# Kernel tuning notes

Hardware: AMD Instinct MI355X
Metric: run time of the kernel (lower is better)

The kernel has to match this reference:

```python
import jax, jax.numpy as jnp
import numpy as np

QMAX = 127.0

def setup_inputs() -> dict:
    key = jax.random.key(0)
    kx, kw, ks = jax.random.split(key, 3)
    B, S, D_IN, D_OUT = 4, 2048, 4096, 4096
    x = jax.random.normal(kx, (B, S, D_IN), dtype=jnp.float16)
    # int8 weight buffer, same distribution as torch.randint(-127, 127)
    weight = jax.random.randint(kw, (D_OUT, D_IN), -127, 127, dtype=jnp.int32).astype(jnp.int8)
    # per-output-channel weight scales (fp16 buffer); small positive values
    weight_scales = (jax.random.uniform(ks, (D_OUT,), dtype=jnp.float32) * 0.01 + 1e-4).astype(jnp.float16)
    return {"x": x, "weight": weight, "weight_scales": weight_scales}

def reference(x, weight, weight_scales):
    # x: [B, S, D_in] fp16; weight: [D_out, D_in] int8; weight_scales: [D_out] fp16
    x32 = x.astype(jnp.float32)
    # dynamic per-token absmax quantization: scale = absmax / 127
    absmax = jnp.max(jnp.abs(x32), axis=-1, keepdims=True)      # [B, S, 1]
    x_scales = jnp.maximum(absmax / QMAX, 1e-8)
    q = jnp.round(x32 / x_scales)                                # in [-127, 127]
    q = jnp.clip(q, -QMAX, QMAX).astype(jnp.int8)
    # int8 GEMM accumulated in int32 (cupy.matmul on int32 in the original)
    y = jnp.einsum('bsk,nk->bsn', q.astype(jnp.int32), weight.astype(jnp.int32),
                   preferred_element_type=jnp.int32)             # [B, S, D_out]
    # dequant: per-token activation scale * per-channel weight scale
    y = y.astype(jnp.float32) * x_scales * weight_scales.astype(jnp.float32)[None, None, :]
    return y.astype(jnp.float16)
```

## Files before the change

kernel.cpp:

```cpp
#include <hip/hip_runtime.h>
#include <stdint.h>

typedef int int32x4 __attribute__((ext_vector_type(4)));

constexpr int K_DIM = 4096;
constexpr int N_DIM = 4096;
constexpr float QMAXF = 127.0f;

__global__ __launch_bounds__(256) void quant_rows(const float* __restrict__ x,
                                                  int8_t* __restrict__ q,
                                                  float* __restrict__ scales) {
    const int row = blockIdx.x;
    const int tid = threadIdx.x;
    const size_t base = (size_t)row * K_DIM;

    const float4* xv = reinterpret_cast<const float4*>(x + base);
    float4 v[4];
#pragma unroll
    for (int i = 0; i < 4; ++i) v[i] = xv[tid + 256 * i];

    float m = 0.0f;
#pragma unroll
    for (int i = 0; i < 4; ++i)
        m = fmaxf(m, fmaxf(fmaxf(fabsf(v[i].x), fabsf(v[i].y)),
                           fmaxf(fabsf(v[i].z), fabsf(v[i].w))));
#pragma unroll
    for (int off = 32; off > 0; off >>= 1) m = fmaxf(m, __shfl_xor(m, off));

    __shared__ float wmax[4];
    if ((tid & 63) == 0) wmax[tid >> 6] = m;
    __syncthreads();
    const float am = fmaxf(fmaxf(wmax[0], wmax[1]), fmaxf(wmax[2], wmax[3]));
    const float scale = fmaxf(am * (1.0f / 127.0f), 1e-8f);
    if (tid == 0) scales[row] = scale;
    const float inv = 1.0f / scale;

    int* qw = reinterpret_cast<int*>(q + base);
#pragma unroll
    for (int i = 0; i < 4; ++i) {
        float f0 = fminf(QMAXF, fmaxf(-QMAXF, rintf(v[i].x * inv)));
        float f1 = fminf(QMAXF, fmaxf(-QMAXF, rintf(v[i].y * inv)));
        float f2 = fminf(QMAXF, fmaxf(-QMAXF, rintf(v[i].z * inv)));
        float f3 = fminf(QMAXF, fmaxf(-QMAXF, rintf(v[i].w * inv)));
        int b0 = ((int)f0) & 255, b1 = ((int)f1) & 255;
        int b2 = ((int)f2) & 255, b3 = ((int)f3) & 255;
        qw[tid + 256 * i] = b0 | (b1 << 8) | (b2 << 16) | (b3 << 24);
    }
}

__global__ __launch_bounds__(256) void pack_w(const int* __restrict__ w,
                                              int8_t* __restrict__ w8) {
    const int idx = blockIdx.x * 256 + threadIdx.x;
    const int4 v = reinterpret_cast<const int4*>(w)[idx];
    int packed = (v.x & 255) | ((v.y & 255) << 8) | ((v.z & 255) << 16) | ((v.w & 255) << 24);
    reinterpret_cast<int*>(w8)[idx] = packed;
}

constexpr int BM = 256, BN = 256, BK = 64;
constexpr int NT = K_DIM / BK;

#define GLL(src, dst)                                                          \
    __builtin_amdgcn_global_load_lds(                                          \
        (const __attribute__((address_space(1))) unsigned int*)(src),          \
        (__attribute__((address_space(3))) unsigned int*)(dst), 16, 0, 0)

__global__ __launch_bounds__(512, 2) void w8a8_gemm256(
        const int8_t* __restrict__ A, const int8_t* __restrict__ B,
        const float* __restrict__ asc, const float* __restrict__ wsc,
        float* __restrict__ C, int M) {
    __shared__ int8_t As[4][BM][BK];
    extern __shared__ int8_t Bs_raw[];
    int8_t* Bs = Bs_raw;

    const int tid  = threadIdx.x;
    const int lane = tid & 63;

    const int nwg = gridDim.x;
    const int bid = blockIdx.x;
    const int swz = (bid & 7) * (nwg >> 3) + (bid >> 3);
    const int NB  = N_DIM / BN;
    const int brow = (swz / NB) * BM;
    const int bcol = (swz % NB) * BN;

    const int wm = (tid >> 6) >> 2;
    const int wn = (tid >> 6) & 3;

    const int s0 = tid, s1 = tid + 512;
    const int r0s = s0 >> 2, g0 = (s0 & 3) ^ ((r0s >> 1) & 3);
    const int r1s = s1 >> 2, g1 = (s1 & 3) ^ ((r1s >> 1) & 3);
    const int8_t* gA0 = A + (size_t)(brow + r0s) * K_DIM + g0 * 16;
    const int8_t* gA1 = A + (size_t)(brow + r1s) * K_DIM + g1 * 16;
    const int8_t* gB0 = B + (size_t)(bcol + r0s) * K_DIM + g0 * 16;
    const int8_t* gB1 = B + (size_t)(bcol + r1s) * K_DIM + g1 * 16;
    const int segb0 = (tid >> 6) * 1024;
    const int segb1 = segb0 + 8192;

    const int l15 = lane & 15;
    const int ls  = lane >> 4;
    const int rA  = wm * 128 + l15;
    const int offA = rA * BK + ((ls ^ ((rA >> 1) & 3)) * 16);
    const int rB  = wn * 64 + l15;
    const int offB = rB * BK + ((ls ^ ((rB >> 1) & 3)) * 16);

    int32x4 acc[8][4];
#pragma unroll
    for (int i = 0; i < 8; ++i)
#pragma unroll
        for (int j = 0; j < 4; ++j) acc[i][j] = (int32x4){0, 0, 0, 0};

#pragma unroll
    for (int t = 0; t < 3; ++t) {
        const size_t kk = (size_t)t * BK;
        int8_t* lA = &As[t][0][0];
        int8_t* lB = Bs + t * (BM * BK);
        GLL(gA0 + kk, lA + segb0);
        GLL(gA1 + kk, lA + segb1);
        GLL(gB0 + kk, lB + segb0);
        GLL(gB1 + kk, lB + segb1);
    }
    asm volatile("s_waitcnt vmcnt(8)" ::: "memory");
    __builtin_amdgcn_s_barrier();

    for (int t = 0; t < NT; ++t) {
        const int b = t & 3;
        const int8_t* abuf = &As[b][0][0];
        const int8_t* bbuf = Bs + b * (BM * BK);
        const int   pb  = (t + 3) & 3;
        const size_t kk = (size_t)(t + 3) * BK;
        const bool  pf  = (t + 3 < NT);

        if (pf) {
            int8_t* lA = &As[pb][0][0];
            GLL(gA0 + kk, lA + segb0);
            GLL(gA1 + kk, lA + segb1);
        }
        int32x4 bf[4], af[4];
#pragma unroll
        for (int ni = 0; ni < 4; ++ni)
            bf[ni] = *(const int32x4*)(bbuf + offB + ni * 1024);
#pragma unroll
        for (int mi = 0; mi < 4; ++mi)
            af[mi] = *(const int32x4*)(abuf + offA + mi * 1024);
        __builtin_amdgcn_s_setprio(1);
#pragma unroll
        for (int mi = 0; mi < 4; ++mi)
#pragma unroll
            for (int ni = 0; ni < 4; ++ni)
                acc[mi][ni] = __builtin_amdgcn_mfma_i32_16x16x64_i8(
                    af[mi], bf[ni], acc[mi][ni], 0, 0, 0);
        __builtin_amdgcn_s_setprio(0);
        __builtin_amdgcn_s_barrier();

        if (pf) {
            int8_t* lB = Bs + pb * (BM * BK);
            GLL(gB0 + kk, lB + segb0);
            GLL(gB1 + kk, lB + segb1);
        }
#pragma unroll
        for (int mi = 0; mi < 4; ++mi)
            af[mi] = *(const int32x4*)(abuf + offA + (mi + 4) * 1024);
        __builtin_amdgcn_s_setprio(1);
#pragma unroll
        for (int mi = 0; mi < 4; ++mi)
#pragma unroll
            for (int ni = 0; ni < 4; ++ni)
                acc[mi + 4][ni] = __builtin_amdgcn_mfma_i32_16x16x64_i8(
                    af[mi], bf[ni], acc[mi + 4][ni], 0, 0, 0);
        __builtin_amdgcn_s_setprio(0);

        if (t < NT - 3)       asm volatile("s_waitcnt vmcnt(8)" ::: "memory");
        else if (t == NT - 3) asm volatile("s_waitcnt vmcnt(4)" ::: "memory");
        else                  asm volatile("s_waitcnt vmcnt(0)" ::: "memory");
        __builtin_amdgcn_s_barrier();
    }

    const int c0  = lane & 15;
    const int rr0 = (lane >> 4) * 4;
#pragma unroll
    for (int ni = 0; ni < 4; ++ni) {
        const int col = bcol + wn * 64 + ni * 16 + c0;
        const float ws = wsc[col];
#pragma unroll
        for (int mi = 0; mi < 8; ++mi) {
            const int rowb = brow + wm * 128 + mi * 16 + rr0;
#pragma unroll
            for (int r = 0; r < 4; ++r) {
                const int row = rowb + r;
                float o = (float)acc[mi][ni][r] * asc[row] * ws;
                o = (float)(_Float16)o;
                C[(size_t)row * N_DIM + col] = o;
            }
        }
    }
}

extern "C" void kernel_launch(void* const* d_in, const int* in_sizes, int n_in,
                              void* d_out, int out_size, void* d_ws, size_t ws_size,
                              hipStream_t stream) {
    const float* x   = (const float*)d_in[0];
    const int*   w   = (const int*)d_in[1];
    const float* wsc = (const float*)d_in[2];
    float* out = (float*)d_out;

    const int K = K_DIM;
    const int M = in_sizes[0] / K;
    const int N = N_DIM;

    int8_t* q   = (int8_t*)d_ws;
    int8_t* w8  = (int8_t*)d_ws + (size_t)M * K;
    float*  asc = (float*)((char*)d_ws + (size_t)M * K + (size_t)N * K);

    quant_rows<<<M, 256, 0, stream>>>(x, q, asc);
    pack_w<<<(N * (K / 4)) / 256, 256, 0, stream>>>(w, w8);
    const int grid = (M / BM) * (N / BN);
    w8a8_gemm256<<<grid, 512, 65536, stream>>>(q, w8, asc, wsc, out, M);
}
```

Before: 199.6 us.

## Split GEMM main loop into four phases with next-tile B fragment prefetch

Restructures the int8 MFMA main loop into four sub-phases per K tile. Each phase issues one global-to-LDS load, reads two A fragments, and prefetches one B fragment from the next stage buffer, then runs eight MFMAs. B fragments are now held in registers across iterations (current and next), and the vmcnt waits are retuned to match. The aim is to spread LDS reads and global loads more evenly between the MFMAs and hide LDS latency. The cost is extra register pressure and eight barriers per K tile instead of two.

```diff
diff --git a/kernel.cpp b/kernel.cpp
--- a/kernel.cpp
+++ b/kernel.cpp
@@ -63,6 +63,8 @@
     __builtin_amdgcn_global_load_lds(                                          \
         (const __attribute__((address_space(1))) unsigned int*)(src),          \
         (__attribute__((address_space(3))) unsigned int*)(dst), 16, 0, 0)
+
+#define MFMA_I8(a, b, c) __builtin_amdgcn_mfma_i32_16x16x64_i8((a), (b), (c), 0, 0, 0)
 
 __global__ __launch_bounds__(512, 2) void w8a8_gemm256(
         const int8_t* __restrict__ A, const int8_t* __restrict__ B,
@@ -118,60 +120,54 @@
         GLL(gB0 + kk, lB + segb0);
         GLL(gB1 + kk, lB + segb1);
     }
-    asm volatile("s_waitcnt vmcnt(8)" ::: "memory");
+    asm volatile("s_waitcnt vmcnt(4)" ::: "memory");
     __builtin_amdgcn_s_barrier();
 
+    int32x4 bf_c[4];
+#pragma unroll
+    for (int p = 0; p < 4; ++p)
+        bf_c[p] = *(const int32x4*)(Bs + offB + p * 1024);
+
     for (int t = 0; t < NT; ++t) {
-        const int b = t & 3;
-        const int8_t* abuf = &As[b][0][0];
-        const int8_t* bbuf = Bs + b * (BM * BK);
-        const int   pb  = (t + 3) & 3;
+        const int8_t* abuf  = &As[t & 3][0][0];
+        const int8_t* bnext = Bs + ((t + 1) & 3) * (BM * BK);
+        int8_t* lA = &As[(t + 3) & 3][0][0];
+        int8_t* lB = Bs + ((t + 3) & 3) * (BM * BK);
         const size_t kk = (size_t)(t + 3) * BK;
-        const bool  pf  = (t + 3 < NT);
-
-        if (pf) {
-            int8_t* lA = &As[pb][0][0];
-            GLL(gA0 + kk, lA + segb0);
-            GLL(gA1 + kk, lA + segb1);
+        const bool pf = (t + 3 < NT);
+
+        int32x4 bf_n[4];
+#pragma unroll
+        for (int p = 0; p < 4; ++p) {
+            if (pf) {
+                if      (p == 0) GLL(gA0 + kk, lA + segb0);
+                else if (p == 1) GLL(gA1 + kk, lA + segb1);
+                else if (p == 2) GLL(gB0 + kk, lB + segb0);
+                else             GLL(gB1 + kk, lB + segb1);
+            }
+            int32x4 a0 = *(const int32x4*)(abuf + offA + (2 * p) * 1024);
+            int32x4 a1 = *(const int32x4*)(abuf + offA + (2 * p + 1) * 1024);
+            bf_n[p]    = *(const int32x4*)(bnext + offB + p * 1024);
+
+            __builtin_amdgcn_s_barrier();
+            asm volatile("s_waitcnt lgkmcnt(0)" ::: "memory");
+            __builtin_amdgcn_s_setprio(1);
+#pragma unroll
+            for (int ni = 0; ni < 4; ++ni)
+                acc[2 * p][ni] = MFMA_I8(a0, bf_c[ni], acc[2 * p][ni]);
+#pragma unroll
+            for (int ni = 0; ni < 4; ++ni)
+                acc[2 * p + 1][ni] = MFMA_I8(a1, bf_c[ni], acc[2 * p + 1][ni]);
+            __builtin_amdgcn_s_setprio(0);
+
+            if (p == 3) {
+                if (t < NT - 3) asm volatile("s_waitcnt vmcnt(4)" ::: "memory");
+                else            asm volatile("s_waitcnt vmcnt(0)" ::: "memory");
+            }
+            __builtin_amdgcn_s_barrier();
         }
-        int32x4 bf[4], af[4];
-#pragma unroll
-        for (int ni = 0; ni < 4; ++ni)
-            bf[ni] = *(const int32x4*)(bbuf + offB + ni * 1024);
-#pragma unroll
-        for (int mi = 0; mi < 4; ++mi)
-            af[mi] = *(const int32x4*)(abuf + offA + mi * 1024);
-        __builtin_amdgcn_s_setprio(1);
-#pragma unroll
-        for (int mi = 0; mi < 4; ++mi)
-#pragma unroll
-            for (int ni = 0; ni < 4; ++ni)
-                acc[mi][ni] = __builtin_amdgcn_mfma_i32_16x16x64_i8(
-                    af[mi], bf[ni], acc[mi][ni], 0, 0, 0);
-        __builtin_amdgcn_s_setprio(0);
-        __builtin_amdgcn_s_barrier();
-
-        if (pf) {
-            int8_t* lB = Bs + pb * (BM * BK);
-            GLL(gB0 + kk, lB + segb0);
-            GLL(gB1 + kk, lB + segb1);
-        }
-#pragma unroll
-        for (int mi = 0; mi < 4; ++mi)
-            af[mi] = *(const int32x4*)(abuf + offA + (mi + 4) * 1024);
-        __builtin_amdgcn_s_setprio(1);
-#pragma unroll
-        for (int mi = 0; mi < 4; ++mi)
-#pragma unroll
-            for (int ni = 0; ni < 4; ++ni)
-                acc[mi + 4][ni] = __builtin_amdgcn_mfma_i32_16x16x64_i8(
-                    af[mi], bf[ni], acc[mi + 4][ni], 0, 0, 0);
-        __builtin_amdgcn_s_setprio(0);
-
-        if (t < NT - 3)       asm volatile("s_waitcnt vmcnt(8)" ::: "memory");
-        else if (t == NT - 3) asm volatile("s_waitcnt vmcnt(4)" ::: "memory");
-        else                  asm volatile("s_waitcnt vmcnt(0)" ::: "memory");
-        __builtin_amdgcn_s_barrier();
+#pragma unroll
+        for (int p = 0; p < 4; ++p) bf_c[p] = bf_n[p];
     }
 
     const int c0  = lane & 15;
```

Result: slower. 206.6 us (+3.5%).

## Load A fragments directly from global into registers, keep only B in LDS

Applied to the files above, without the earlier changes.

The GEMM no longer stages the activation tile in LDS. Each wave loads its A fragments straight from global memory into registers, double-buffered one K-step ahead, while B stays in a 3-stage LDS ring filled by global_load_lds. This removes the A LDS traffic and its 64KB of dynamic shared memory and shrinks LDS use per block. In exchange each wave issues more global loads without sharing them (A rows are loaded once per wn wave, four times total) and uses more registers for the A prefetch buffers. The vmcnt wait accounting is hand-tuned.

```diff
diff --git a/kernel.cpp b/kernel.cpp
--- a/kernel.cpp
+++ b/kernel.cpp
@@ -64,16 +64,17 @@
         (const __attribute__((address_space(1))) unsigned int*)(src),          \
         (__attribute__((address_space(3))) unsigned int*)(dst), 16, 0, 0)
 
+#define MFMA_I8(a, b, c) __builtin_amdgcn_mfma_i32_16x16x64_i8((a), (b), (c), 0, 0, 0)
+
 __global__ __launch_bounds__(512, 2) void w8a8_gemm256(
         const int8_t* __restrict__ A, const int8_t* __restrict__ B,
         const float* __restrict__ asc, const float* __restrict__ wsc,
         float* __restrict__ C, int M) {
-    __shared__ int8_t As[4][BM][BK];
-    extern __shared__ int8_t Bs_raw[];
-    int8_t* Bs = Bs_raw;
+    __shared__ int8_t Bs[3][BM][BK];
 
     const int tid  = threadIdx.x;
     const int lane = tid & 63;
+    const int wave = tid >> 6;
 
     const int nwg = gridDim.x;
     const int bid = blockIdx.x;
@@ -82,96 +83,106 @@
     const int brow = (swz / NB) * BM;
     const int bcol = (swz % NB) * BN;
 
-    const int wm = (tid >> 6) >> 2;
-    const int wn = (tid >> 6) & 3;
+    const int wm = wave >> 2;
+    const int wn = wave & 3;
+
+    const int l15 = lane & 15;
+    const int ls  = lane >> 4;
 
     const int s0 = tid, s1 = tid + 512;
     const int r0s = s0 >> 2, g0 = (s0 & 3) ^ ((r0s >> 1) & 3);
     const int r1s = s1 >> 2, g1 = (s1 & 3) ^ ((r1s >> 1) & 3);
-    const int8_t* gA0 = A + (size_t)(brow + r0s) * K_DIM + g0 * 16;
-    const int8_t* gA1 = A + (size_t)(brow + r1s) * K_DIM + g1 * 16;
     const int8_t* gB0 = B + (size_t)(bcol + r0s) * K_DIM + g0 * 16;
     const int8_t* gB1 = B + (size_t)(bcol + r1s) * K_DIM + g1 * 16;
-    const int segb0 = (tid >> 6) * 1024;
+    const int segb0 = wave * 1024;
     const int segb1 = segb0 + 8192;
 
-    const int l15 = lane & 15;
-    const int ls  = lane >> 4;
-    const int rA  = wm * 128 + l15;
-    const int offA = rA * BK + ((ls ^ ((rA >> 1) & 3)) * 16);
     const int rB  = wn * 64 + l15;
     const int offB = rB * BK + ((ls ^ ((rB >> 1) & 3)) * 16);
 
+    const int8_t* aptr = A + (size_t)(brow + wm * 128 + l15) * K_DIM + ls * 16;
+
     int32x4 acc[8][4];
 #pragma unroll
     for (int i = 0; i < 8; ++i)
 #pragma unroll
         for (int j = 0; j < 4; ++j) acc[i][j] = (int32x4){0, 0, 0, 0};
 
-#pragma unroll
-    for (int t = 0; t < 3; ++t) {
-        const size_t kk = (size_t)t * BK;
-        int8_t* lA = &As[t][0][0];
-        int8_t* lB = Bs + t * (BM * BK);
-        GLL(gA0 + kk, lA + segb0);
-        GLL(gA1 + kk, lA + segb1);
-        GLL(gB0 + kk, lB + segb0);
-        GLL(gB1 + kk, lB + segb1);
-    }
-    asm volatile("s_waitcnt vmcnt(8)" ::: "memory");
+    int32x4 av0[8], av1[8];
+
+#pragma unroll
+    for (int mi = 0; mi < 8; ++mi)
+        av0[mi] = *(const int32x4*)(aptr + (size_t)mi * 16 * K_DIM);
+    GLL(gB0, &Bs[0][0][0] + segb0);
+    GLL(gB1, &Bs[0][0][0] + segb1);
+    GLL(gB0 + 64, &Bs[1][0][0] + segb0);
+    GLL(gB1 + 64, &Bs[1][0][0] + segb1);
+    asm volatile("s_waitcnt vmcnt(2)" ::: "memory");
     __builtin_amdgcn_s_barrier();
 
-    for (int t = 0; t < NT; ++t) {
-        const int b = t & 3;
-        const int8_t* abuf = &As[b][0][0];
-        const int8_t* bbuf = Bs + b * (BM * BK);
-        const int   pb  = (t + 3) & 3;
-        const size_t kk = (size_t)(t + 3) * BK;
-        const bool  pf  = (t + 3 < NT);
-
-        if (pf) {
-            int8_t* lA = &As[pb][0][0];
-            GLL(gA0 + kk, lA + segb0);
-            GLL(gA1 + kk, lA + segb1);
-        }
-        int32x4 bf[4], af[4];
+#define BODY_FULL(T, CUR, NXT)                                                 \
+    {                                                                          \
+        const int8_t* ap = aptr + ((T) + 1) * 64;                              \
+        _Pragma("unroll")                                                      \
+        for (int mi = 0; mi < 8; ++mi)                                         \
+            NXT[mi] = *(const int32x4*)(ap + (size_t)mi * 16 * K_DIM);         \
+        int8_t* lB = &Bs[((T) + 2) % 3][0][0];                                 \
+        GLL(gB0 + ((T) + 2) * 64, lB + segb0);                                 \
+        GLL(gB1 + ((T) + 2) * 64, lB + segb1);                                 \
+        const int8_t* bbuf = &Bs[(T) % 3][0][0];                               \
+        int32x4 bf[4];                                                         \
+        _Pragma("unroll")                                                      \
+        for (int ni = 0; ni < 4; ++ni)                                         \
+            bf[ni] = *(const int32x4*)(bbuf + offB + ni * 1024);               \
+        __builtin_amdgcn_s_setprio(1);                                         \
+        _Pragma("unroll")                                                      \
+        for (int mi = 0; mi < 8; ++mi)                                         \
+            _Pragma("unroll")                                                  \
+            for (int ni = 0; ni < 4; ++ni)                                     \
+                acc[mi][ni] = MFMA_I8(CUR[mi], bf[ni], acc[mi][ni]);           \
+        __builtin_amdgcn_s_setprio(0);                                         \
+        asm volatile("s_waitcnt vmcnt(10)" ::: "memory");                      \
+        __builtin_amdgcn_s_barrier();                                          \
+    }
+
+    for (int t = 0; t < NT - 2; t += 2) {
+        BODY_FULL(t,     av0, av1);
+        BODY_FULL(t + 1, av1, av0);
+    }
+
+    {
+        const int8_t* ap = aptr + (NT - 1) * 64;
+#pragma unroll
+        for (int mi = 0; mi < 8; ++mi)
+            av1[mi] = *(const int32x4*)(ap + (size_t)mi * 16 * K_DIM);
+        const int8_t* bbuf = &Bs[(NT - 2) % 3][0][0];
+        int32x4 bf[4];
 #pragma unroll
         for (int ni = 0; ni < 4; ++ni)
             bf[ni] = *(const int32x4*)(bbuf + offB + ni * 1024);
-#pragma unroll
-        for (int mi = 0; mi < 4; ++mi)
-            af[mi] = *(const int32x4*)(abuf + offA + mi * 1024);
         __builtin_amdgcn_s_setprio(1);
 #pragma unroll
-        for (int mi = 0; mi < 4; ++mi)
+        for (int mi = 0; mi < 8; ++mi)
 #pragma unroll
             for (int ni = 0; ni < 4; ++ni)
-                acc[mi][ni] = __builtin_amdgcn_mfma_i32_16x16x64_i8(
-                    af[mi], bf[ni], acc[mi][ni], 0, 0, 0);
+                acc[mi][ni] = MFMA_I8(av0[mi], bf[ni], acc[mi][ni]);
         __builtin_amdgcn_s_setprio(0);
+        asm volatile("s_waitcnt vmcnt(8)" ::: "memory");
         __builtin_amdgcn_s_barrier();
-
-        if (pf) {
-            int8_t* lB = Bs + pb * (BM * BK);
-            GLL(gB0 + kk, lB + segb0);
-            GLL(gB1 + kk, lB + segb1);
-        }
-#pragma unroll
-        for (int mi = 0; mi < 4; ++mi)
-            af[mi] = *(const int32x4*)(abuf + offA + (mi + 4) * 1024);
+    }
+    {
+        const int8_t* bbuf = &Bs[(NT - 1) % 3][0][0];
+        int32x4 bf[4];
+#pragma unroll
+        for (int ni = 0; ni < 4; ++ni)
+            bf[ni] = *(const int32x4*)(bbuf + offB + ni * 1024);
         __builtin_amdgcn_s_setprio(1);
 #pragma unroll
-        for (int mi = 0; mi < 4; ++mi)
+        for (int mi = 0; mi < 8; ++mi)
 #pragma unroll
             for (int ni = 0; ni < 4; ++ni)
-                acc[mi + 4][ni] = __builtin_amdgcn_mfma_i32_16x16x64_i8(
-                    af[mi], bf[ni], acc[mi + 4][ni], 0, 0, 0);
+                acc[mi][ni] = MFMA_I8(av1[mi], bf[ni], acc[mi][ni]);
         __builtin_amdgcn_s_setprio(0);
-
-        if (t < NT - 3)       asm volatile("s_waitcnt vmcnt(8)" ::: "memory");
-        else if (t == NT - 3) asm volatile("s_waitcnt vmcnt(4)" ::: "memory");
-        else                  asm volatile("s_waitcnt vmcnt(0)" ::: "memory");
-        __builtin_amdgcn_s_barrier();
     }
 
     const int c0  = lane & 15;
@@ -213,5 +224,5 @@
     quant_rows<<<M, 256, 0, stream>>>(x, q, asc);
     pack_w<<<(N * (K / 4)) / 256, 256, 0, stream>>>(w, w8);
     const int grid = (M / BM) * (N / BN);
-    w8a8_gemm256<<<grid, 512, 65536, stream>>>(q, w8, asc, wsc, out, M);
-}
+    w8a8_gemm256<<<grid, 512, 0, stream>>>(q, w8, asc, wsc, out, M);
+}
```

Measured after the change: 364.9 us. 1.83x slower.

## Double-buffer BK=128 tiles and interleave chunked loads across four MFMA phases

Applied to the files above, without the earlier changes.

The GEMM moves from a 4-stage ring of BK=64 tiles to a 2-stage double buffer of BK=128 tiles in 128KB of dynamic LDS. The swizzle changes to an 8-way XOR. Each K-step's global-to-LDS loads are split into 64-row chunks and spread across four MFMA phases. Waitcnt and barrier points are placed so each chunk lands before the phase that reads it. The aim is fewer loop iterations and barriers per byte, with memory traffic hidden behind more MFMA work, at the cost of a shallower prefetch depth and tighter, fragile vmcnt ordering.

```diff
diff --git a/kernel.cpp b/kernel.cpp
--- a/kernel.cpp
+++ b/kernel.cpp
@@ -56,24 +56,25 @@
     reinterpret_cast<int*>(w8)[idx] = packed;
 }
 
-constexpr int BM = 256, BN = 256, BK = 64;
-constexpr int NT = K_DIM / BK;
+constexpr int BM = 256, BN = 256, BKB = 128;
+constexpr int NT = K_DIM / BKB;
 
 #define GLL(src, dst)                                                          \
     __builtin_amdgcn_global_load_lds(                                          \
         (const __attribute__((address_space(1))) unsigned int*)(src),          \
         (__attribute__((address_space(3))) unsigned int*)(dst), 16, 0, 0)
 
+#define MFMA_I8(a, b, c) __builtin_amdgcn_mfma_i32_16x16x64_i8((a), (b), (c), 0, 0, 0)
+
 __global__ __launch_bounds__(512, 2) void w8a8_gemm256(
         const int8_t* __restrict__ A, const int8_t* __restrict__ B,
         const float* __restrict__ asc, const float* __restrict__ wsc,
         float* __restrict__ C, int M) {
-    __shared__ int8_t As[4][BM][BK];
-    extern __shared__ int8_t Bs_raw[];
-    int8_t* Bs = Bs_raw;
+    extern __shared__ int8_t lds[];
 
     const int tid  = threadIdx.x;
     const int lane = tid & 63;
+    const int wave = tid >> 6;
 
     const int nwg = gridDim.x;
     const int bid = blockIdx.x;
@@ -82,25 +83,21 @@
     const int brow = (swz / NB) * BM;
     const int bcol = (swz % NB) * BN;
 
-    const int wm = (tid >> 6) >> 2;
-    const int wn = (tid >> 6) & 3;
-
-    const int s0 = tid, s1 = tid + 512;
-    const int r0s = s0 >> 2, g0 = (s0 & 3) ^ ((r0s >> 1) & 3);
-    const int r1s = s1 >> 2, g1 = (s1 & 3) ^ ((r1s >> 1) & 3);
-    const int8_t* gA0 = A + (size_t)(brow + r0s) * K_DIM + g0 * 16;
-    const int8_t* gA1 = A + (size_t)(brow + r1s) * K_DIM + g1 * 16;
-    const int8_t* gB0 = B + (size_t)(bcol + r0s) * K_DIM + g0 * 16;
-    const int8_t* gB1 = B + (size_t)(bcol + r1s) * K_DIM + g1 * 16;
-    const int segb0 = (tid >> 6) * 1024;
-    const int segb1 = segb0 + 8192;
-
+    const int wm = wave >> 2;
+    const int wn = wave & 3;
     const int l15 = lane & 15;
     const int ls  = lane >> 4;
-    const int rA  = wm * 128 + l15;
-    const int offA = rA * BK + ((ls ^ ((rA >> 1) & 3)) * 16);
-    const int rB  = wn * 64 + l15;
-    const int offB = rB * BK + ((ls ^ ((rB >> 1) & 3)) * 16);
+
+    const int rowin = tid >> 3;
+    const int gsl   = ((tid & 7) ^ (rowin & 7)) * 16;
+    const int8_t* gA = A + (size_t)(brow + rowin) * K_DIM + gsl;
+    const int8_t* gB = B + (size_t)(bcol + rowin) * K_DIM + gsl;
+    const size_t chunk_g = (size_t)64 * K_DIM;
+    const int segb = wave * 1024;
+
+    const int sbase = ((ls ^ (l15 & 7)) * 16);
+    const int offA0 = (wm * 128 + l15) * BKB + sbase;
+    const int offB0 = (wn * 64  + l15) * BKB + sbase;
 
     int32x4 acc[8][4];
 #pragma unroll
@@ -109,68 +106,109 @@
         for (int j = 0; j < 4; ++j) acc[i][j] = (int32x4){0, 0, 0, 0};
 
 #pragma unroll
-    for (int t = 0; t < 3; ++t) {
-        const size_t kk = (size_t)t * BK;
-        int8_t* lA = &As[t][0][0];
-        int8_t* lB = Bs + t * (BM * BK);
-        GLL(gA0 + kk, lA + segb0);
-        GLL(gA1 + kk, lA + segb1);
-        GLL(gB0 + kk, lB + segb0);
-        GLL(gB1 + kk, lB + segb1);
-    }
-    asm volatile("s_waitcnt vmcnt(8)" ::: "memory");
+    for (int c = 0; c < 4; ++c) {
+        GLL(gA + c * chunk_g, lds + c * 8192 + segb);
+        GLL(gB + c * chunk_g, lds + 65536 + c * 8192 + segb);
+    }
+    asm volatile("s_waitcnt vmcnt(0)" ::: "memory");
     __builtin_amdgcn_s_barrier();
 
+    int32x4 af[8], bf01[4], bf23[4];
+
     for (int t = 0; t < NT; ++t) {
-        const int b = t & 3;
-        const int8_t* abuf = &As[b][0][0];
-        const int8_t* bbuf = Bs + b * (BM * BK);
-        const int   pb  = (t + 3) & 3;
-        const size_t kk = (size_t)(t + 3) * BK;
-        const bool  pf  = (t + 3 < NT);
+        const int8_t* Ab = lds + (t & 1) * 32768;
+        const int8_t* Bb = lds + 65536 + (t & 1) * 32768;
+        const int  p1   = (t + 1) & 1;
+        const bool pf   = (t + 1 < NT);
+        const size_t kk = (size_t)(t + 1) * BKB;
+        int8_t* dA = lds + p1 * 32768;
+        int8_t* dB = lds + 65536 + p1 * 32768;
 
         if (pf) {
-            int8_t* lA = &As[pb][0][0];
-            GLL(gA0 + kk, lA + segb0);
-            GLL(gA1 + kk, lA + segb1);
-        }
-        int32x4 bf[4], af[4];
-#pragma unroll
-        for (int ni = 0; ni < 4; ++ni)
-            bf[ni] = *(const int32x4*)(bbuf + offB + ni * 1024);
-#pragma unroll
-        for (int mi = 0; mi < 4; ++mi)
-            af[mi] = *(const int32x4*)(abuf + offA + mi * 1024);
-        __builtin_amdgcn_s_setprio(1);
-#pragma unroll
-        for (int mi = 0; mi < 4; ++mi)
-#pragma unroll
-            for (int ni = 0; ni < 4; ++ni)
-                acc[mi][ni] = __builtin_amdgcn_mfma_i32_16x16x64_i8(
-                    af[mi], bf[ni], acc[mi][ni], 0, 0, 0);
-        __builtin_amdgcn_s_setprio(0);
+            GLL(gA + kk,               dA + segb);
+            GLL(gA + kk + 2 * chunk_g, dA + 16384 + segb);
+            GLL(gB + kk,               dB + segb);
+        }
+#pragma unroll
+        for (int mi = 0; mi < 4; ++mi) {
+            af[2 * mi]     = *(const int32x4*)(Ab + ((offA0 + mi * 2048)));
+            af[2 * mi + 1] = *(const int32x4*)(Ab + ((offA0 + mi * 2048) ^ 64));
+        }
+#pragma unroll
+        for (int ni = 0; ni < 2; ++ni) {
+            bf01[2 * ni]     = *(const int32x4*)(Bb + ((offB0 + ni * 2048)));
+            bf01[2 * ni + 1] = *(const int32x4*)(Bb + ((offB0 + ni * 2048) ^ 64));
+        }
+        __builtin_amdgcn_s_barrier();
+        asm volatile("s_waitcnt lgkmcnt(0)" ::: "memory");
+        __builtin_amdgcn_s_setprio(1);
+#pragma unroll
+        for (int mi = 0; mi < 4; ++mi)
+#pragma unroll
+            for (int ni = 0; ni < 2; ++ni)
+#pragma unroll
+                for (int kh = 0; kh < 2; ++kh)
+                    acc[mi][ni] = MFMA_I8(af[2 * mi + kh], bf01[2 * ni + kh], acc[mi][ni]);
+        __builtin_amdgcn_s_setprio(0);
+        if (t < NT - 1) asm volatile("s_waitcnt vmcnt(3)" ::: "memory");
+        else            asm volatile("s_waitcnt vmcnt(0)" ::: "memory");
         __builtin_amdgcn_s_barrier();
 
         if (pf) {
-            int8_t* lB = Bs + pb * (BM * BK);
-            GLL(gB0 + kk, lB + segb0);
-            GLL(gB1 + kk, lB + segb1);
-        }
-#pragma unroll
-        for (int mi = 0; mi < 4; ++mi)
-            af[mi] = *(const int32x4*)(abuf + offA + (mi + 4) * 1024);
-        __builtin_amdgcn_s_setprio(1);
-#pragma unroll
-        for (int mi = 0; mi < 4; ++mi)
-#pragma unroll
-            for (int ni = 0; ni < 4; ++ni)
-                acc[mi + 4][ni] = __builtin_amdgcn_mfma_i32_16x16x64_i8(
-                    af[mi], bf[ni], acc[mi + 4][ni], 0, 0, 0);
-        __builtin_amdgcn_s_setprio(0);
-
-        if (t < NT - 3)       asm volatile("s_waitcnt vmcnt(8)" ::: "memory");
-        else if (t == NT - 3) asm volatile("s_waitcnt vmcnt(4)" ::: "memory");
-        else                  asm volatile("s_waitcnt vmcnt(0)" ::: "memory");
+            GLL(gB + kk + 1 * chunk_g, dB + 8192 + segb);
+            GLL(gB + kk + 2 * chunk_g, dB + 16384 + segb);
+            GLL(gB + kk + 3 * chunk_g, dB + 24576 + segb);
+        }
+#pragma unroll
+        for (int ni = 0; ni < 2; ++ni) {
+            bf23[2 * ni]     = *(const int32x4*)(Bb + ((offB0 + (ni + 2) * 2048)));
+            bf23[2 * ni + 1] = *(const int32x4*)(Bb + ((offB0 + (ni + 2) * 2048) ^ 64));
+        }
+        __builtin_amdgcn_s_barrier();
+        asm volatile("s_waitcnt lgkmcnt(0)" ::: "memory");
+        __builtin_amdgcn_s_setprio(1);
+#pragma unroll
+        for (int mi = 0; mi < 4; ++mi)
+#pragma unroll
+            for (int ni = 0; ni < 2; ++ni)
+#pragma unroll
+                for (int kh = 0; kh < 2; ++kh)
+                    acc[mi][ni + 2] = MFMA_I8(af[2 * mi + kh], bf23[2 * ni + kh], acc[mi][ni + 2]);
+        __builtin_amdgcn_s_setprio(0);
+        __builtin_amdgcn_s_barrier();
+
+        if (pf) {
+            GLL(gA + kk + 1 * chunk_g, dA + 8192 + segb);
+            GLL(gA + kk + 3 * chunk_g, dA + 24576 + segb);
+        }
+#pragma unroll
+        for (int mi = 0; mi < 4; ++mi) {
+            af[2 * mi]     = *(const int32x4*)(Ab + ((offA0 + (mi + 4) * 2048)));
+            af[2 * mi + 1] = *(const int32x4*)(Ab + ((offA0 + (mi + 4) * 2048) ^ 64));
+        }
+        __builtin_amdgcn_s_barrier();
+        asm volatile("s_waitcnt lgkmcnt(0)" ::: "memory");
+        __builtin_amdgcn_s_setprio(1);
+#pragma unroll
+        for (int mi = 0; mi < 4; ++mi)
+#pragma unroll
+            for (int ni = 0; ni < 2; ++ni)
+#pragma unroll
+                for (int kh = 0; kh < 2; ++kh)
+                    acc[mi + 4][ni + 2] = MFMA_I8(af[2 * mi + kh], bf23[2 * ni + kh], acc[mi + 4][ni + 2]);
+        __builtin_amdgcn_s_setprio(0);
+        __builtin_amdgcn_s_barrier();
+
+        __builtin_amdgcn_s_setprio(1);
+#pragma unroll
+        for (int mi = 0; mi < 4; ++mi)
+#pragma unroll
+            for (int ni = 0; ni < 2; ++ni)
+#pragma unroll
+                for (int kh = 0; kh < 2; ++kh)
+                    acc[mi + 4][ni] = MFMA_I8(af[2 * mi + kh], bf01[2 * ni + kh], acc[mi + 4][ni]);
+        __builtin_amdgcn_s_setprio(0);
+        asm volatile("s_waitcnt vmcnt(2)" ::: "memory");
         __builtin_amdgcn_s_barrier();
     }
 
@@ -213,5 +251,5 @@
     quant_rows<<<M, 256, 0, stream>>>(x, q, asc);
     pack_w<<<(N * (K / 4)) / 256, 256, 0, stream>>>(w, w8);
     const int grid = (M / BM) * (N / BN);
-    w8a8_gemm256<<<grid, 512, 65536, stream>>>(q, w8, asc, wsc, out, M);
-}
+    w8a8_gemm256<<<grid, 512, 131072, stream>>>(q, w8, asc, wsc, out, M);
+}
```

New measurement: 186.2 us. 6.7% less time.
